# Performance work log

Measured on AMD Instinct MI355X. Metric: run time of the kernel, lower is better.

The kernel has to match this reference:

```python
import jax, jax.numpy as jnp
import numpy as np

B, T, K = 16, 512, 128  # batch, seq_len, num_state


def setup_inputs() -> dict:
    key = jax.random.key(0)
    k1, k2, k3 = jax.random.split(key, 3)
    transition = jax.random.normal(k1, (K, K), dtype=jnp.float32)
    emission = jax.random.normal(k2, (B, T, K), dtype=jnp.float32)
    seq_lens = jax.random.randint(k3, (B,), 1, T + 1)  # lengths in [1, T]
    return {"transition": transition, "emission": emission, "seq_lens": seq_lens}


def reference(transition, emission, seq_lens):
    # potential_normalization='none' -> identity normalize().
    # combine_potentials: log phi[b, t, y_{t-1}, y_t] = trans[y_{t-1}, y_t] + emis[b, t, y_t]
    log_pot = transition[None, None, :, :] + emission[:, :, None, :]  # [B,T,K,K]

    alpha0 = emission[:, 0, :]  # [B,K]

    def step(alpha_prev, pot_t):  # alpha_prev: [B,K], pot_t: [B,K,K]
        alpha_t = jax.nn.logsumexp(alpha_prev[:, :, None] + pot_t, axis=1)
        return alpha_t, alpha_t

    # scan over time steps 1..T-1 (time-major potentials)
    _, alphas_rest = jax.lax.scan(step, alpha0, jnp.swapaxes(log_pot[:, 1:], 0, 1))
    alpha = jnp.concatenate(
        [alpha0[:, None, :], jnp.swapaxes(alphas_rest, 0, 1)], axis=1
    )  # [B,T,K]

    # gather alpha at position seq_lens - 1 per batch element
    last = jnp.take_along_axis(alpha, (seq_lens - 1)[:, None, None], axis=1)[:, 0, :]
    log_Z = jax.nn.logsumexp(last, axis=-1)  # [B]
    return alpha, log_Z
```

## Files before the change

kernel.cpp:

```cpp
#include <hip/hip_runtime.h>
#include <math.h>

#define KDIM 128
#define TLEN 512
#define BATCH 16
#define CH_L 16
#define NCH 32
#define NMAT 31

typedef _Float16 half8 __attribute__((ext_vector_type(8)));
typedef _Float16 half4 __attribute__((ext_vector_type(4)));
typedef _Float16 half2t __attribute__((ext_vector_type(2)));
typedef float floatx4 __attribute__((ext_vector_type(4)));

#if defined(__has_builtin)
#if __has_builtin(__builtin_amdgcn_fdot2)
#define HAVE_FDOT2 1
#endif
#endif

static __device__ __forceinline__ float dot2f(half2t a, half2t b, float c) {
#ifdef HAVE_FDOT2
    return __builtin_amdgcn_fdot2(a, b, c, false);
#else
    return fmaf((float)a[0], (float)b[0], fmaf((float)a[1], (float)b[1], c));
#endif
}

#define WS_PST   0
#define WS_ETA   16252928
#define WS_ETB   16285696
#define WS_SLOG  16320512
#define WS_AENT  16322496
#define WS_MT    16584640
#define WS_NEED  16584644


__global__ __launch_bounds__(256) void crf_prep2(const float* __restrict__ trans,
                                                 _Float16* __restrict__ EtA,
                                                 _Float16* __restrict__ EtB,
                                                 float* __restrict__ mTout)
{
    const int tid = threadIdx.x;
    __shared__ float slot[4];
    __shared__ __align__(16) _Float16 sb[17408];

    float mt = -INFINITY;
    for (int s = 0; s < 64; ++s) mt = fmaxf(mt, trans[tid + s * 256]);
    #pragma unroll
    for (int o = 32; o; o >>= 1) mt = fmaxf(mt, __shfl_xor(mt, o));
    if ((tid & 63) == 0) slot[tid >> 6] = mt;
    __syncthreads();
    const float mT = fmaxf(fmaxf(slot[0], slot[1]), fmaxf(slot[2], slot[3]));

    for (int s = 0; s < 64; ++s) {
        int e = tid + s * 256;
        int k = e >> 7, m = e & 127;
        float v = __expf(trans[e] - mT);
        sb[((((m >> 4) * 4 + (k >> 5)) * 4 + ((k >> 3) & 3)) * 16 + (m & 15)) * 8 + (k & 7)] =
            (_Float16)v;
    }
    __syncthreads();
    for (int s = 0; s < 8; ++s) {
        int x = (tid + s * 256) * 8;
        *(half8*)&EtA[x] = *(const half8*)&sb[x];
    }
    __syncthreads();

    for (int s = 0; s < 64; ++s) {
        int e = tid + s * 256;
        int i = e >> 7, j = e & 127;
        float v = __expf(trans[e] - mT);
        sb[((i >> 4) * 16 + (j >> 3)) * 136 + (i & 15) * 8 + (j & 7)] = (_Float16)v;
    }
    __syncthreads();
    for (int s = 0; s < 9; ++s) {
        int g = tid + s * 256;
        if (g < 2176) {
            int x = g * 8;
            *(half8*)&EtB[x] = *(const half8*)&sb[x];
        }
    }
    if (tid == 0) mTout[0] = mT;
}

__global__ __launch_bounds__(256, 2) void crf_chunkmat3(
    const float* __restrict__ em,
    const _Float16* __restrict__ EtA, const _Float16* __restrict__ EtB,
    const float* __restrict__ mTws,
    _Float16* __restrict__ Pst, float* __restrict__ Sout)
{
    const int c = blockIdx.x;
    const int b = blockIdx.y;
    const int tid = threadIdx.x;
    const int w = tid >> 6, lane = tid & 63;
    const int quad = lane >> 4, lm = lane & 15;

    __shared__ __align__(16) _Float16 buf[17408];
    __shared__ __align__(16) float gAll[16 * KDIM];
    __shared__ float mE[16];
    __shared__ float slotV[4];

    const float mT = mTws[0];
    const int t0 = c * CH_L + 1;
    const float* emb = em + (size_t)b * TLEN * KDIM;

    half8 EA[2][4];
    #pragma unroll
    for (int r = 0; r < 2; ++r) {
        const int tr = 2 * w + r;
        #pragma unroll
        for (int kt = 0; kt < 4; ++kt)
            EA[r][kt] = *(const half8*)&EtA[(((tr * 4 + kt) * 4 + quad) * 16 + lm) * 8];
    }

    #pragma unroll
    for (int s = 0; s < 2; ++s) {
        int i4 = tid + s * 256;
        *(float4*)&gAll[i4 * 4] = *(const float4*)&emb[t0 * KDIM + i4 * 4];
    }
    __syncthreads();

    #pragma unroll
    for (int r2 = 0; r2 < 4; ++r2) {
        const int r = w * 4 + r2;
        float v = fmaxf(gAll[r * KDIM + lane], gAll[r * KDIM + 64 + lane]);
        #pragma unroll
        for (int o = 32; o; o >>= 1) v = fmaxf(v, __shfl_xor(v, o));
        if (lane == 0) mE[r] = v;
    }
    __syncthreads();

    #pragma unroll
    for (int s = 0; s < 8; ++s) {
        int idx = tid + s * 256;
        gAll[idx] = __expf(gAll[idx] - mE[idx >> 7]);
    }
    __syncthreads();

    for (int s = 0; s < 8; ++s) {
        int g = tid + s * 256;
        int row = g >> 4, nl = g & 15;
        int addr = row * 136 + nl * 8;
        int j0 = (row & 15) * 8;
        half8 e = *(const half8*)&EtB[addr];
        const float* g0p = &gAll[j0];
        half8 o;
        #pragma unroll
        for (int x = 0; x < 8; ++x) o[x] = (_Float16)((float)e[x] * g0p[x]);
        *(half8*)&buf[addr] = o;
    }
    float S = mT;
    if (tid == 0) {
        #pragma unroll
        for (int r = 0; r < 16; ++r) S += mE[r];
    }
    __syncthreads();

    floatx4 acc[2][8];

    for (int it = 1; it < 16; ++it) {
        #pragma unroll
        for (int r = 0; r < 2; ++r)
            #pragma unroll
            for (int nt = 0; nt < 8; ++nt)
                acc[r][nt] = (floatx4){0.f, 0.f, 0.f, 0.f};

        #pragma unroll
        for (int kt = 0; kt < 4; ++kt) {
            #pragma unroll
            for (int nt = 0; nt < 8; ++nt) {
                half8 bb = *(const half8*)&buf[(nt * 16 + kt * 4 + quad) * 136 + lm * 8];
                acc[0][nt] = __builtin_amdgcn_mfma_f32_16x16x32_f16(EA[0][kt], bb, acc[0][nt], 0, 0, 0);
                acc[1][nt] = __builtin_amdgcn_mfma_f32_16x16x32_f16(EA[1][kt], bb, acc[1][nt], 0, 0, 0);
            }
        }

        const float* gc = &gAll[it * KDIM];
        const float4 gr0 = *(const float4*)&gc[(2 * w + 0) * 16 + quad * 4];
        const float4 gr1 = *(const float4*)&gc[(2 * w + 1) * 16 + quad * 4];

        float lmax = 0.f;
        #pragma unroll
        for (int nt = 0; nt < 8; ++nt) {
            floatx4 v0 = acc[0][nt], v1 = acc[1][nt];
            float a0 = fmaxf(fmaxf(v0.x * gr0.x, v0.y * gr0.y), fmaxf(v0.z * gr0.z, v0.w * gr0.w));
            float a1 = fmaxf(fmaxf(v1.x * gr1.x, v1.y * gr1.y), fmaxf(v1.z * gr1.z, v1.w * gr1.w));
            lmax = fmaxf(lmax, fmaxf(a0, a1));
        }
        #pragma unroll
        for (int o = 32; o; o >>= 1) lmax = fmaxf(lmax, __shfl_xor(lmax, o));
        if (lane == 0) slotV[w] = lmax;
        __syncthreads();

        const float rr = fmaxf(fmaxf(slotV[0], slotV[1]), fmaxf(slotV[2], slotV[3]));
        const float rinv = 1.0f / rr;
        if (tid == 0) S += mT + __logf(rr);

        const float4 s0 = {gr0.x * rinv, gr0.y * rinv, gr0.z * rinv, gr0.w * rinv};
        const float4 s1 = {gr1.x * rinv, gr1.y * rinv, gr1.z * rinv, gr1.w * rinv};
        const int jlb = (quad & 1) * 4;
        #pragma unroll
        for (int r = 0; r < 2; ++r) {
            const int tr = 2 * w + r;
            const int kh = tr * 2 + (quad >> 1);
            const float4 sc = r ? s1 : s0;
            #pragma unroll
            for (int nt = 0; nt < 8; ++nt) {
                const floatx4 v = acc[r][nt];
                half4 o;
                o[0] = (_Float16)(v.x * sc.x);
                o[1] = (_Float16)(v.y * sc.y);
                o[2] = (_Float16)(v.z * sc.z);
                o[3] = (_Float16)(v.w * sc.w);
                *(half4*)&buf[(nt * 16 + kh) * 136 + lm * 8 + jlb] = o;
            }
        }
        __syncthreads();
    }

    _Float16* Pc = Pst + ((size_t)(b * NMAT + c)) * 16384;
    for (int s = 0; s < 8; ++s) {
        int u = tid + s * 256;
        int K = u >> 7, j = u & 127;
        const int base = ((K >> 1) * 16 + (j >> 3)) * 136 + (j & 7);
        const int eoff = (K & 1) * 64;
        half8 v;
        #pragma unroll
        for (int e = 0; e < 8; ++e) v[e] = buf[base + eoff + e * 8];
        *(half8*)&Pc[u * 8] = v;
    }
    if (tid == 0) Sout[b * NMAT + c] = S;
}

__global__ __launch_bounds__(64, 1) void crf_scanw(
    const float* __restrict__ em, const _Float16* __restrict__ Pst,
    const float* __restrict__ S, float* __restrict__ aEnter)
{
    const int b = blockIdx.x;
    const int lane = threadIdx.x;
    const int j0 = 2 * lane;

    __shared__ __align__(16) _Float16 pbuf[KDIM];
    __shared__ float Sl[NMAT];

    const _Float16* Pb = Pst + (size_t)b * NMAT * 16384;
    float* aeb = aEnter + (size_t)b * NCH * KDIM;

    if (lane < NMAT) Sl[lane] = S[b * NMAT + lane];

    float2 a0 = *(const float2*)&em[(size_t)b * TLEN * KDIM + j0];
    float mx = fmaxf(a0.x, a0.y);
    #pragma unroll
    for (int o = 32; o; o >>= 1) mx = fmaxf(mx, __shfl_xor(mx, o));
    float L = mx;
    *(float2*)&aeb[j0] = a0;
    {
        half2t p2;
        p2[0] = (_Float16)__expf(a0.x - L);
        p2[1] = (_Float16)__expf(a0.y - L);
        ((half2t*)pbuf)[lane] = p2;
    }

    half8 PA[2][16], PB[2][16];
    {
        const _Float16* Pc = Pb;
        #pragma unroll
        for (int K = 0; K < 16; ++K) {
            PA[0][K] = *(const half8*)&Pc[(K * 128 + j0) * 8];
            PA[1][K] = *(const half8*)&Pc[(K * 128 + j0) * 8 + 8];
        }
    }

    auto step = [&](const half8 (&P)[2][16], int c) {
        float q0 = 0.f, q1 = 0.f;
        #pragma unroll
        for (int K = 0; K < 16; ++K) {
            const float4 w = *(const float4*)&pbuf[K * 8];
            const half2t pw0 = __builtin_bit_cast(half2t, w.x);
            const half2t pw1 = __builtin_bit_cast(half2t, w.y);
            const half2t pw2 = __builtin_bit_cast(half2t, w.z);
            const half2t pw3 = __builtin_bit_cast(half2t, w.w);
            const half2t* c0 = (const half2t*)&P[0][K];
            const half2t* c1 = (const half2t*)&P[1][K];
            q0 = dot2f(pw0, c0[0], q0); q0 = dot2f(pw1, c0[1], q0);
            q0 = dot2f(pw2, c0[2], q0); q0 = dot2f(pw3, c0[3], q0);
            q1 = dot2f(pw0, c1[0], q1); q1 = dot2f(pw1, c1[1], q1);
            q1 = dot2f(pw2, c1[2], q1); q1 = dot2f(pw3, c1[3], q1);
        }
        const float s_c = Sl[c];
        const float sigma = __shfl(q0, 0);
        const float base = L + s_c;
        float2 st;
        st.x = base + __logf(q0);
        st.y = base + __logf(q1);
        *(float2*)&aeb[(c + 1) * KDIM + j0] = st;
        const float ri = 1.0f / sigma;
        half2t p2;
        p2[0] = (_Float16)(q0 * ri);
        p2[1] = (_Float16)(q1 * ri);
        ((half2t*)pbuf)[lane] = p2;
        L = base + __logf(sigma);
    };

    for (int c = 0; c < NMAT; c += 2) {
        if (c + 1 < NMAT) {
            const _Float16* Pc = Pb + (size_t)(c + 1) * 16384;
            #pragma unroll
            for (int K = 0; K < 16; ++K) {
                PB[0][K] = *(const half8*)&Pc[(K * 128 + j0) * 8];
                PB[1][K] = *(const half8*)&Pc[(K * 128 + j0) * 8 + 8];
            }
        }
        step(PA, c);
        if (c + 1 < NMAT) {
            if (c + 2 < NMAT) {
                const _Float16* Pc = Pb + (size_t)(c + 2) * 16384;
                #pragma unroll
                for (int K = 0; K < 16; ++K) {
                    PA[0][K] = *(const half8*)&Pc[(K * 128 + j0) * 8];
                    PA[1][K] = *(const half8*)&Pc[(K * 128 + j0) * 8 + 8];
                }
            }
            step(PB, c + 1);
        }
    }
}

__global__ __launch_bounds__(64, 1) void crf_replayw(
    const float* __restrict__ trans, const float* __restrict__ em,
    const int* __restrict__ seq_lens, const float* __restrict__ aEnter,
    float* __restrict__ alpha, float* __restrict__ logZ)
{
    const int c = blockIdx.x, b = blockIdx.y;
    const int l = threadIdx.x;

    __shared__ __align__(16) _Float16 pbuf[KDIM];

    half2t Ea[64], Eb[64];
    #pragma unroll
    for (int t2 = 0; t2 < 64; ++t2) {
        const float* r0 = &trans[(2 * t2) * KDIM];
        const float* r1 = &trans[(2 * t2 + 1) * KDIM];
        half2t ea, eb;
        ea[0] = (_Float16)__expf(r0[l]);
        ea[1] = (_Float16)__expf(r1[l]);
        eb[0] = (_Float16)__expf(r0[l + 64]);
        eb[1] = (_Float16)__expf(r1[l + 64]);
        Ea[t2] = ea;
        Eb[t2] = eb;
    }

    const int len = seq_lens[b];
    const float* emb = em + (size_t)b * TLEN * KDIM;
    float* outb = alpha + (size_t)b * TLEN * KDIM;
    const float* ae = aEnter + ((size_t)b * NCH + c) * KDIM;

    float a0 = ae[l], a1 = ae[l + 64];
    float mx = fmaxf(a0, a1);
    #pragma unroll
    for (int o = 32; o; o >>= 1) mx = fmaxf(mx, __shfl_xor(mx, o));
    float L = mx;
    pbuf[l]      = (_Float16)__expf(a0 - L);
    pbuf[l + 64] = (_Float16)__expf(a1 - L);

    float la0 = 0.f, la1 = -INFINITY;
    if (c == 0) {
        outb[l] = a0;
        outb[l + 64] = a1;
        if (len == 1) { la0 = a0; la1 = a1; }
    }

    const int t_begin = c * CH_L + 1;
    const int t_end = (c == NCH - 1) ? (TLEN - 1) : (c * CH_L + CH_L);

    float e0 = emb[t_begin * KDIM + l];
    float e1 = emb[t_begin * KDIM + l + 64];

    for (int t = t_begin; t <= t_end; ++t) {
        float n0 = 0.f, n1 = 0.f;
        if (t < t_end) {
            n0 = emb[(t + 1) * KDIM + l];
            n1 = emb[(t + 1) * KDIM + l + 64];
        }

        float q0 = 0.f, q1 = 0.f;
        #pragma unroll
        for (int s = 0; s < 16; ++s) {
            const float4 w = *(const float4*)&pbuf[s * 8];
            const half2t p0 = __builtin_bit_cast(half2t, w.x);
            const half2t p1 = __builtin_bit_cast(half2t, w.y);
            const half2t p2 = __builtin_bit_cast(half2t, w.z);
            const half2t p3 = __builtin_bit_cast(half2t, w.w);
            q0 = dot2f(p0, Ea[4 * s + 0], q0);
            q0 = dot2f(p1, Ea[4 * s + 1], q0);
            q0 = dot2f(p2, Ea[4 * s + 2], q0);
            q0 = dot2f(p3, Ea[4 * s + 3], q0);
            q1 = dot2f(p0, Eb[4 * s + 0], q1);
            q1 = dot2f(p1, Eb[4 * s + 1], q1);
            q1 = dot2f(p2, Eb[4 * s + 2], q1);
            q1 = dot2f(p3, Eb[4 * s + 3], q1);
        }

        const float A0 = e0 + L + __logf(q0);
        const float A1 = e1 + L + __logf(q1);
        outb[t * KDIM + l] = A0;
        outb[t * KDIM + l + 64] = A1;
        if (t == len - 1) { la0 = A0; la1 = A1; }

        const float sigma = __shfl(q0, 0);
        const float ri = 1.0f / sigma;
        pbuf[l]      = (_Float16)(q0 * ri * __expf(e0));
        pbuf[l + 64] = (_Float16)(q1 * ri * __expf(e1));
        L += __logf(sigma);
        e0 = n0; e1 = n1;
    }

    const bool blockowns = (len == 1) ? (c == 0) : (((len - 2) >> 4) == c);
    if (blockowns) {
        float m2 = fmaxf(la0, la1);
        #pragma unroll
        for (int o = 32; o; o >>= 1) m2 = fmaxf(m2, __shfl_xor(m2, o));
        float e = __expf(la0 - m2) + __expf(la1 - m2);
        #pragma unroll
        for (int o = 32; o; o >>= 1) e += __shfl_xor(e, o);
        if (l == 0) logZ[b] = m2 + __logf(e);
    }
}

__global__ __launch_bounds__(256) void crf_forward_fallback(
    const float* __restrict__ trans, const float* __restrict__ em,
    const int* __restrict__ seq_lens, float* __restrict__ alpha_out,
    float* __restrict__ logZ_out)
{
    const int b = blockIdx.x;
    const int tid = threadIdx.x;
    const int j = tid & (KDIM - 1);
    const int h = tid >> 7;

    __shared__ __align__(16) float p_lds[KDIM];
    __shared__ float part[KDIM];
    __shared__ float red[8];

    float Ereg[64];
    #pragma unroll
    for (int k = 0; k < 64; ++k) Ereg[k] = __expf(trans[(h * 64 + k) * KDIM + j]);

    const int len = seq_lens[b];
    const float* emb = em + (size_t)b * TLEN * KDIM;
    float* outb = alpha_out + (size_t)b * TLEN * KDIM;

    float a = 0.f, last_a = 0.f;
    if (h == 0) {
        a = emb[j];
        outb[j] = a;
        if (len == 1) last_a = a;
    }
    for (int t = 1; t < TLEN; ++t) {
        {
            float v = (h == 0) ? a : -INFINITY;
            #pragma unroll
            for (int o = 32; o >= 1; o >>= 1) v = fmaxf(v, __shfl_xor(v, o));
            if ((tid & 63) == 0) red[tid >> 6] = v;
        }
        __syncthreads();
        const float m = fmaxf(red[0], red[1]);
        if (h == 0) p_lds[j] = __expf(a - m);
        __syncthreads();
        float em_t = 0.f;
        if (h == 0) em_t = emb[t * KDIM + j];
        float acc0 = 0.f, acc1 = 0.f, acc2 = 0.f, acc3 = 0.f;
        const float4* p4 = (const float4*)(p_lds + h * 64);
        #pragma unroll
        for (int k4 = 0; k4 < 16; ++k4) {
            float4 pv = p4[k4];
            acc0 = fmaf(pv.x, Ereg[4 * k4 + 0], acc0);
            acc1 = fmaf(pv.y, Ereg[4 * k4 + 1], acc1);
            acc2 = fmaf(pv.z, Ereg[4 * k4 + 2], acc2);
            acc3 = fmaf(pv.w, Ereg[4 * k4 + 3], acc3);
        }
        const float acc = (acc0 + acc1) + (acc2 + acc3);
        if (h == 1) part[j] = acc;
        __syncthreads();
        if (h == 0) {
            const float q = acc + part[j];
            a = em_t + m + __logf(q);
            outb[t * KDIM + j] = a;
            if (t == len - 1) last_a = a;
        }
    }
    {
        float v = (h == 0) ? last_a : -INFINITY;
        #pragma unroll
        for (int o = 32; o >= 1; o >>= 1) v = fmaxf(v, __shfl_xor(v, o));
        if ((tid & 63) == 0) red[tid >> 6] = v;
    }
    __syncthreads();
    const float m2 = fmaxf(red[0], red[1]);
    float e = (h == 0) ? __expf(last_a - m2) : 0.f;
    #pragma unroll
    for (int o = 32; o >= 1; o >>= 1) e += __shfl_xor(e, o);
    if ((tid & 63) == 0) red[4 + (tid >> 6)] = e;
    __syncthreads();
    if (tid == 0) logZ_out[b] = m2 + logf(red[4] + red[5]);
}

extern "C" void kernel_launch(void* const* d_in, const int* in_sizes, int n_in,
                              void* d_out, int out_size, void* d_ws, size_t ws_size,
                              hipStream_t stream) {
    const float* trans    = (const float*)d_in[0];
    const float* em       = (const float*)d_in[1];
    const int*   seq_lens = (const int*)d_in[2];

    float* alpha_out = (float*)d_out;
    float* logZ_out  = alpha_out + (size_t)BATCH * TLEN * KDIM;

    if (ws_size < (size_t)WS_NEED) {
        crf_forward_fallback<<<BATCH, 256, 0, stream>>>(trans, em, seq_lens,
                                                        alpha_out, logZ_out);
        return;
    }

    char* ws = (char*)d_ws;
    _Float16* Pst  = (_Float16*)(ws + WS_PST);
    _Float16* EtA  = (_Float16*)(ws + WS_ETA);
    _Float16* EtB  = (_Float16*)(ws + WS_ETB);
    float*    Slog = (float*)(ws + WS_SLOG);
    float*    aEnt = (float*)(ws + WS_AENT);
    float*    mTws = (float*)(ws + WS_MT);

    crf_prep2<<<1, 256, 0, stream>>>(trans, EtA, EtB, mTws);
    crf_chunkmat3<<<dim3(NMAT, BATCH), 256, 0, stream>>>(em, EtA, EtB, mTws, Pst, Slog);
    crf_scanw<<<BATCH, 64, 0, stream>>>(em, Pst, Slog, aEnt);
    crf_replayw<<<dim3(NCH, BATCH), 64, 0, stream>>>(trans, em, seq_lens, aEnt,
                                                     alpha_out, logZ_out);
}
```

Measured before the change: 175.2 us.

## Fuse prep into chunk kernel and overlap scan with replay via flags

Drops the separate transition-prep kernel: each chunk-matrix block now computes exp(trans) itself without max-subtraction, which removes a launch and a global round trip but adds redundant exp work and a risk of fp16 overflow for large transition values. The scan and replay kernels are merged into one launch. Scan blocks publish each chunk's entry alpha and set a per-chunk flag, and replay blocks spin on that flag so they can start as soon as their chunk is ready instead of waiting for the whole scan. This relies on the scan blocks being scheduled alongside the spinning blocks (their lower block indices should dispatch first). Flags are reset by block (0,0) of the previous kernel.

After: 179.2 us. 1.02x slower.

```diff
diff --git a/kernel.cpp b/kernel.cpp
--- a/kernel.cpp
+++ b/kernel.cpp
@@ -28,67 +28,16 @@
 }
 
 #define WS_PST   0
-#define WS_ETA   16252928
-#define WS_ETB   16285696
-#define WS_SLOG  16320512
-#define WS_AENT  16322496
-#define WS_MT    16584640
-#define WS_NEED  16584644
-
-
-__global__ __launch_bounds__(256) void crf_prep2(const float* __restrict__ trans,
-                                                 _Float16* __restrict__ EtA,
-                                                 _Float16* __restrict__ EtB,
-                                                 float* __restrict__ mTout)
-{
-    const int tid = threadIdx.x;
-    __shared__ float slot[4];
-    __shared__ __align__(16) _Float16 sb[17408];
-
-    float mt = -INFINITY;
-    for (int s = 0; s < 64; ++s) mt = fmaxf(mt, trans[tid + s * 256]);
-    #pragma unroll
-    for (int o = 32; o; o >>= 1) mt = fmaxf(mt, __shfl_xor(mt, o));
-    if ((tid & 63) == 0) slot[tid >> 6] = mt;
-    __syncthreads();
-    const float mT = fmaxf(fmaxf(slot[0], slot[1]), fmaxf(slot[2], slot[3]));
-
-    for (int s = 0; s < 64; ++s) {
-        int e = tid + s * 256;
-        int k = e >> 7, m = e & 127;
-        float v = __expf(trans[e] - mT);
-        sb[((((m >> 4) * 4 + (k >> 5)) * 4 + ((k >> 3) & 3)) * 16 + (m & 15)) * 8 + (k & 7)] =
-            (_Float16)v;
-    }
-    __syncthreads();
-    for (int s = 0; s < 8; ++s) {
-        int x = (tid + s * 256) * 8;
-        *(half8*)&EtA[x] = *(const half8*)&sb[x];
-    }
-    __syncthreads();
-
-    for (int s = 0; s < 64; ++s) {
-        int e = tid + s * 256;
-        int i = e >> 7, j = e & 127;
-        float v = __expf(trans[e] - mT);
-        sb[((i >> 4) * 16 + (j >> 3)) * 136 + (i & 15) * 8 + (j & 7)] = (_Float16)v;
-    }
-    __syncthreads();
-    for (int s = 0; s < 9; ++s) {
-        int g = tid + s * 256;
-        if (g < 2176) {
-            int x = g * 8;
-            *(half8*)&EtB[x] = *(const half8*)&sb[x];
-        }
-    }
-    if (tid == 0) mTout[0] = mT;
-}
-
-__global__ __launch_bounds__(256, 2) void crf_chunkmat3(
-    const float* __restrict__ em,
-    const _Float16* __restrict__ EtA, const _Float16* __restrict__ EtB,
-    const float* __restrict__ mTws,
-    _Float16* __restrict__ Pst, float* __restrict__ Sout)
+#define WS_SLOG  16252928
+#define WS_AENT  16254912
+#define WS_FLAG  16517056
+#define WS_NEED  16519104
+
+
+__global__ __launch_bounds__(256, 2) void crf_chunkmat4(
+    const float* __restrict__ trans, const float* __restrict__ em,
+    _Float16* __restrict__ Pst, float* __restrict__ Sout,
+    unsigned* __restrict__ flags)
 {
     const int c = blockIdx.x;
     const int b = blockIdx.y;
@@ -101,17 +50,25 @@
     __shared__ float mE[16];
     __shared__ float slotV[4];
 
-    const float mT = mTws[0];
+    if (c == 0 && b == 0) {
+        flags[tid] = 0u;
+        flags[tid + 256] = 0u;
+    }
+
     const int t0 = c * CH_L + 1;
     const float* emb = em + (size_t)b * TLEN * KDIM;
 
     half8 EA[2][4];
     #pragma unroll
     for (int r = 0; r < 2; ++r) {
-        const int tr = 2 * w + r;
-        #pragma unroll
-        for (int kt = 0; kt < 4; ++kt)
-            EA[r][kt] = *(const half8*)&EtA[(((tr * 4 + kt) * 4 + quad) * 16 + lm) * 8];
+        const int m = (2 * w + r) * 16 + lm;
+        #pragma unroll
+        for (int kt = 0; kt < 4; ++kt) {
+            #pragma unroll
+            for (int i = 0; i < 8; ++i) {
+                EA[r][kt][i] = (_Float16)__expf(trans[(kt * 32 + quad * 8 + i) * KDIM + m]);
+            }
+        }
     }
 
     #pragma unroll
@@ -142,15 +99,17 @@
         int g = tid + s * 256;
         int row = g >> 4, nl = g & 15;
         int addr = row * 136 + nl * 8;
-        int j0 = (row & 15) * 8;
-        half8 e = *(const half8*)&EtB[addr];
+        int koct = row & 15;
+        int n = (row >> 4) * 16 + nl;
+        int j0 = koct * 8;
+        const float* tr_ = &trans[n * KDIM + j0];
         const float* g0p = &gAll[j0];
         half8 o;
         #pragma unroll
-        for (int x = 0; x < 8; ++x) o[x] = (_Float16)((float)e[x] * g0p[x]);
+        for (int x = 0; x < 8; ++x) o[x] = (_Float16)(__expf(tr_[x]) * g0p[x]);
         *(half8*)&buf[addr] = o;
     }
-    float S = mT;
+    float S = 0.f;
     if (tid == 0) {
         #pragma unroll
         for (int r = 0; r < 16; ++r) S += mE[r];
@@ -195,7 +154,7 @@
 
         const float rr = fmaxf(fmaxf(slotV[0], slotV[1]), fmaxf(slotV[2], slotV[3]));
         const float rinv = 1.0f / rr;
-        if (tid == 0) S += mT + __logf(rr);
+        if (tid == 0) S += __logf(rr);
 
         const float4 s0 = {gr0.x * rinv, gr0.y * rinv, gr0.z * rinv, gr0.w * rinv};
         const float4 s1 = {gr1.x * rinv, gr1.y * rinv, gr1.z * rinv, gr1.w * rinv};
@@ -233,109 +192,112 @@
     if (tid == 0) Sout[b * NMAT + c] = S;
 }
 
-__global__ __launch_bounds__(64, 1) void crf_scanw(
-    const float* __restrict__ em, const _Float16* __restrict__ Pst,
-    const float* __restrict__ S, float* __restrict__ aEnter)
+__global__ __launch_bounds__(64, 1) void crf_tail(
+    const float* __restrict__ trans, const float* __restrict__ em,
+    const int* __restrict__ seq_lens,
+    const _Float16* __restrict__ Pst, const float* __restrict__ S,
+    float* __restrict__ aEnter, unsigned* __restrict__ flags,
+    float* __restrict__ alpha, float* __restrict__ logZ)
 {
-    const int b = blockIdx.x;
+    const int gb = blockIdx.x;
     const int lane = threadIdx.x;
-    const int j0 = 2 * lane;
 
     __shared__ __align__(16) _Float16 pbuf[KDIM];
     __shared__ float Sl[NMAT];
 
-    const _Float16* Pb = Pst + (size_t)b * NMAT * 16384;
-    float* aeb = aEnter + (size_t)b * NCH * KDIM;
-
-    if (lane < NMAT) Sl[lane] = S[b * NMAT + lane];
-
-    float2 a0 = *(const float2*)&em[(size_t)b * TLEN * KDIM + j0];
-    float mx = fmaxf(a0.x, a0.y);
-    #pragma unroll
-    for (int o = 32; o; o >>= 1) mx = fmaxf(mx, __shfl_xor(mx, o));
-    float L = mx;
-    *(float2*)&aeb[j0] = a0;
-    {
-        half2t p2;
-        p2[0] = (_Float16)__expf(a0.x - L);
-        p2[1] = (_Float16)__expf(a0.y - L);
-        ((half2t*)pbuf)[lane] = p2;
-    }
-
-    half8 PA[2][16], PB[2][16];
-    {
-        const _Float16* Pc = Pb;
-        #pragma unroll
-        for (int K = 0; K < 16; ++K) {
-            PA[0][K] = *(const half8*)&Pc[(K * 128 + j0) * 8];
-            PA[1][K] = *(const half8*)&Pc[(K * 128 + j0) * 8 + 8];
-        }
-    }
-
-    auto step = [&](const half8 (&P)[2][16], int c) {
-        float q0 = 0.f, q1 = 0.f;
-        #pragma unroll
-        for (int K = 0; K < 16; ++K) {
-            const float4 w = *(const float4*)&pbuf[K * 8];
-            const half2t pw0 = __builtin_bit_cast(half2t, w.x);
-            const half2t pw1 = __builtin_bit_cast(half2t, w.y);
-            const half2t pw2 = __builtin_bit_cast(half2t, w.z);
-            const half2t pw3 = __builtin_bit_cast(half2t, w.w);
-            const half2t* c0 = (const half2t*)&P[0][K];
-            const half2t* c1 = (const half2t*)&P[1][K];
-            q0 = dot2f(pw0, c0[0], q0); q0 = dot2f(pw1, c0[1], q0);
-            q0 = dot2f(pw2, c0[2], q0); q0 = dot2f(pw3, c0[3], q0);
-            q1 = dot2f(pw0, c1[0], q1); q1 = dot2f(pw1, c1[1], q1);
-            q1 = dot2f(pw2, c1[2], q1); q1 = dot2f(pw3, c1[3], q1);
-        }
-        const float s_c = Sl[c];
-        const float sigma = __shfl(q0, 0);
-        const float base = L + s_c;
-        float2 st;
-        st.x = base + __logf(q0);
-        st.y = base + __logf(q1);
-        *(float2*)&aeb[(c + 1) * KDIM + j0] = st;
-        const float ri = 1.0f / sigma;
-        half2t p2;
-        p2[0] = (_Float16)(q0 * ri);
-        p2[1] = (_Float16)(q1 * ri);
-        ((half2t*)pbuf)[lane] = p2;
-        L = base + __logf(sigma);
-    };
-
-    for (int c = 0; c < NMAT; c += 2) {
-        if (c + 1 < NMAT) {
-            const _Float16* Pc = Pb + (size_t)(c + 1) * 16384;
+    if (gb < BATCH) {
+        const int b = gb;
+        const int j0 = 2 * lane;
+        const _Float16* Pb = Pst + (size_t)b * NMAT * 16384;
+        float* aeb = aEnter + (size_t)b * NCH * KDIM;
+        unsigned* fl = flags + b * NCH;
+
+        if (lane < NMAT) Sl[lane] = S[b * NMAT + lane];
+
+        float2 a0 = *(const float2*)&em[(size_t)b * TLEN * KDIM + j0];
+        float mx = fmaxf(a0.x, a0.y);
+        #pragma unroll
+        for (int o = 32; o; o >>= 1) mx = fmaxf(mx, __shfl_xor(mx, o));
+        float L = mx;
+        *(float2*)&aeb[j0] = a0;
+        {
+            half2t p2;
+            p2[0] = (_Float16)__expf(a0.x - L);
+            p2[1] = (_Float16)__expf(a0.y - L);
+            ((half2t*)pbuf)[lane] = p2;
+        }
+
+        half8 PA[2][16], PB[2][16];
+        {
+            const _Float16* Pc = Pb;
             #pragma unroll
             for (int K = 0; K < 16; ++K) {
-                PB[0][K] = *(const half8*)&Pc[(K * 128 + j0) * 8];
-                PB[1][K] = *(const half8*)&Pc[(K * 128 + j0) * 8 + 8];
-            }
-        }
-        step(PA, c);
-        if (c + 1 < NMAT) {
-            if (c + 2 < NMAT) {
-                const _Float16* Pc = Pb + (size_t)(c + 2) * 16384;
+                PA[0][K] = *(const half8*)&Pc[(K * 128 + j0) * 8];
+                PA[1][K] = *(const half8*)&Pc[(K * 128 + j0) * 8 + 8];
+            }
+        }
+
+        auto step = [&](const half8 (&P)[2][16], int c) {
+            float q0 = 0.f, q1 = 0.f;
+            #pragma unroll
+            for (int K = 0; K < 16; ++K) {
+                const float4 w = *(const float4*)&pbuf[K * 8];
+                const half2t pw0 = __builtin_bit_cast(half2t, w.x);
+                const half2t pw1 = __builtin_bit_cast(half2t, w.y);
+                const half2t pw2 = __builtin_bit_cast(half2t, w.z);
+                const half2t pw3 = __builtin_bit_cast(half2t, w.w);
+                const half2t* c0 = (const half2t*)&P[0][K];
+                const half2t* c1 = (const half2t*)&P[1][K];
+                q0 = dot2f(pw0, c0[0], q0); q0 = dot2f(pw1, c0[1], q0);
+                q0 = dot2f(pw2, c0[2], q0); q0 = dot2f(pw3, c0[3], q0);
+                q1 = dot2f(pw0, c1[0], q1); q1 = dot2f(pw1, c1[1], q1);
+                q1 = dot2f(pw2, c1[2], q1); q1 = dot2f(pw3, c1[3], q1);
+            }
+            const float s_c = Sl[c];
+            const float sigma = __shfl(q0, 0);
+            const float base = L + s_c;
+            float2 st;
+            st.x = base + __logf(q0);
+            st.y = base + __logf(q1);
+            *(float2*)&aeb[(c + 1) * KDIM + j0] = st;
+            __threadfence();
+            if (lane == 0) atomicExch(&fl[c + 1], 1u);
+            const float ri = 1.0f / sigma;
+            half2t p2;
+            p2[0] = (_Float16)(q0 * ri);
+            p2[1] = (_Float16)(q1 * ri);
+            ((half2t*)pbuf)[lane] = p2;
+            L = base + __logf(sigma);
+        };
+
+        for (int c = 0; c < NMAT; c += 2) {
+            if (c + 1 < NMAT) {
+                const _Float16* Pc = Pb + (size_t)(c + 1) * 16384;
                 #pragma unroll
                 for (int K = 0; K < 16; ++K) {
-                    PA[0][K] = *(const half8*)&Pc[(K * 128 + j0) * 8];
-                    PA[1][K] = *(const half8*)&Pc[(K * 128 + j0) * 8 + 8];
+                    PB[0][K] = *(const half8*)&Pc[(K * 128 + j0) * 8];
+                    PB[1][K] = *(const half8*)&Pc[(K * 128 + j0) * 8 + 8];
                 }
             }
-            step(PB, c + 1);
-        }
-    }
-}
-
-__global__ __launch_bounds__(64, 1) void crf_replayw(
-    const float* __restrict__ trans, const float* __restrict__ em,
-    const int* __restrict__ seq_lens, const float* __restrict__ aEnter,
-    float* __restrict__ alpha, float* __restrict__ logZ)
-{
-    const int c = blockIdx.x, b = blockIdx.y;
-    const int l = threadIdx.x;
-
-    __shared__ __align__(16) _Float16 pbuf[KDIM];
+            step(PA, c);
+            if (c + 1 < NMAT) {
+                if (c + 2 < NMAT) {
+                    const _Float16* Pc = Pb + (size_t)(c + 2) * 16384;
+                    #pragma unroll
+                    for (int K = 0; K < 16; ++K) {
+                        PA[0][K] = *(const half8*)&Pc[(K * 128 + j0) * 8];
+                        PA[1][K] = *(const half8*)&Pc[(K * 128 + j0) * 8 + 8];
+                    }
+                }
+                step(PB, c + 1);
+            }
+        }
+        return;
+    }
+
+    const int idx = gb - BATCH;
+    const int c = idx & (NCH - 1), b = idx >> 5;
+    const int l = lane;
 
     half2t Ea[64], Eb[64];
     #pragma unroll
@@ -354,9 +316,20 @@
     const int len = seq_lens[b];
     const float* emb = em + (size_t)b * TLEN * KDIM;
     float* outb = alpha + (size_t)b * TLEN * KDIM;
-    const float* ae = aEnter + ((size_t)b * NCH + c) * KDIM;
-
-    float a0 = ae[l], a1 = ae[l + 64];
+
+    float a0, a1;
+    if (c == 0) {
+        a0 = emb[l];
+        a1 = emb[l + 64];
+    } else {
+        unsigned* fp = flags + b * NCH + c;
+        while (atomicAdd(fp, 0u) == 0u) __builtin_amdgcn_s_sleep(32);
+        __threadfence();
+        const float* ae = aEnter + ((size_t)b * NCH + c) * KDIM;
+        a0 = ae[l];
+        a1 = ae[l + 64];
+    }
+
     float mx = fmaxf(a0, a1);
     #pragma unroll
     for (int o = 32; o; o >>= 1) mx = fmaxf(mx, __shfl_xor(mx, o));
@@ -523,15 +496,11 @@
 
     char* ws = (char*)d_ws;
     _Float16* Pst  = (_Float16*)(ws + WS_PST);
-    _Float16* EtA  = (_Float16*)(ws + WS_ETA);
-    _Float16* EtB  = (_Float16*)(ws + WS_ETB);
     float*    Slog = (float*)(ws + WS_SLOG);
     float*    aEnt = (float*)(ws + WS_AENT);
-    float*    mTws = (float*)(ws + WS_MT);
-
-    crf_prep2<<<1, 256, 0, stream>>>(trans, EtA, EtB, mTws);
-    crf_chunkmat3<<<dim3(NMAT, BATCH), 256, 0, stream>>>(em, EtA, EtB, mTws, Pst, Slog);
-    crf_scanw<<<BATCH, 64, 0, stream>>>(em, Pst, Slog, aEnt);
-    crf_replayw<<<dim3(NCH, BATCH), 64, 0, stream>>>(trans, em, seq_lens, aEnt,
-                                                     alpha_out, logZ_out);
+    unsigned* flag = (unsigned*)(ws + WS_FLAG);
+
+    crf_chunkmat4<<<dim3(NMAT, BATCH), 256, 0, stream>>>(trans, em, Pst, Slog, flag);
+    crf_tail<<<BATCH + NCH * BATCH, 64, 0, stream>>>(trans, em, seq_lens, Pst, Slog,
+                                                     aEnt, flag, alpha_out, logZ_out);
 }
```
